# Kernel optimization log

Measured on AMD Instinct MI355X. Metric: run time of the kernel, lower is better.

The kernel has to match this reference:

```python
import jax, jax.numpy as jnp
import numpy as np

DIM = 64
CTX_DIM = 128
B, D, H, W = 4, 64, 64, 64


def setup_inputs() -> dict:
    key = jax.random.key(0)
    ks = jax.random.split(key, 8)
    s_x = 1.0 / np.sqrt(DIM)
    s_c = 1.0 / np.sqrt(CTX_DIM)
    return {
        "x": jax.random.normal(ks[0], (B, DIM, D, H, W), dtype=jnp.float32),
        "context": jax.random.normal(ks[1], (B, CTX_DIM, D, H, W), dtype=jnp.float32),
        # 1x1x1 Conv3d weights flattened to [out_ch, in_ch] plus bias [out_ch]
        "wq": jax.random.uniform(ks[2], (DIM, DIM), jnp.float32, -s_x, s_x),
        "bq": jax.random.uniform(ks[3], (DIM,), jnp.float32, -s_x, s_x),
        "wk": jax.random.uniform(ks[4], (DIM, CTX_DIM), jnp.float32, -s_c, s_c),
        "bk": jax.random.uniform(ks[5], (DIM,), jnp.float32, -s_c, s_c),
        "wv": jax.random.uniform(ks[6], (DIM, CTX_DIM), jnp.float32, -s_c, s_c),
        "bv": jax.random.uniform(ks[7], (DIM,), jnp.float32, -s_c, s_c),
    }


def reference(x, context, wq, bq, wk, bk, wv, bv):
    # 1x1x1 Conv3d == per-voxel channel GEMM
    def conv1(w, b, t):
        return jnp.einsum('oc,bcdhw->bodhw', w, t) + b[None, :, None, None, None]

    scale = x.shape[1] ** (-0.5)
    q = conv1(wq, bq, x)          # [B, dim, D, H, W]
    k = conv1(wk, bk, context)    # [B, dim, D, H, W]
    v = conv1(wv, bv, context)    # [B, dim, D, H, W]

    # (q*scale) @ k^T batched over (B, dim, D): [H,W] @ [W,H] -> [H,H]
    attn = jnp.einsum('bcdhw,bcdgw->bcdhg', q * scale, k)  # [B, dim, D, H, H]
    attn = jax.nn.softmax(attn, axis=-1)
    out = jnp.einsum('bcdhg,bcdgw->bcdhw', attn, v)        # [B, dim, D, H, W]
    return out + x
```

## Files before the change

kernel.cpp:

```cpp
#include <hip/hip_runtime.h>
#include <hip/hip_bf16.h>

typedef short short8 __attribute__((ext_vector_type(8)));
typedef float floatx4 __attribute__((ext_vector_type(4)));
typedef unsigned short ushort_t;

#define NB   4
#define NC_X 64
#define NC_C 128
#define ND   64
#define NHW  4096
#define NH   64
#define NW   64
#define NS   (NB * ND)

__device__ __forceinline__ ushort_t f2bf(float f) {
    unsigned u;
    __builtin_memcpy(&u, &f, 4);
    u += 0x7fffu + ((u >> 16) & 1u);
    return (ushort_t)(u >> 16);
}

__global__ void prep_kernel(const float* __restrict__ wq, const float* __restrict__ bq,
                            const float* __restrict__ wk, const float* __restrict__ bk,
                            const float* __restrict__ wv, const float* __restrict__ bv,
                            ushort_t* __restrict__ wW, float* __restrict__ wB) {
    int t = blockIdx.x * blockDim.x + threadIdx.x;
    int N = gridDim.x * blockDim.x;
    for (int i = t; i < 4096; i += N) wW[i] = f2bf(wq[i] * 0.125f);
    for (int i = t; i < 8192; i += N) wW[4096 + i] = f2bf(wk[i]);
    for (int i = t; i < 8192; i += N) wW[12288 + i] = f2bf(wv[i]);
    for (int i = t; i < 64; i += N) {
        wB[i] = bq[i] * 0.125f;
        wB[64 + i] = bk[i];
        wB[128 + i] = bv[i];
    }
}

__global__ __launch_bounds__(256, 2)
void proj_kernel(const float* __restrict__ x, const float* __restrict__ ctx,
                 const ushort_t* __restrict__ wW, const float* __restrict__ wB,
                 ushort_t* __restrict__ qws, ushort_t* __restrict__ kws,
                 ushort_t* __restrict__ vws, int s0, int nd) {
    __shared__ ushort_t Xs[128][72];
    __shared__ ushort_t Cs[128][136];

    const int t = threadIdx.x;
    const int chunk = blockIdx.x;
    const int si = blockIdx.y;
    const int s = s0 + si;
    const int b = s >> 6;
    const int d = s & 63;
    const int hw0 = chunk * 128;

    const float* xb = x + ((size_t)(b * NC_X) * ND + d) * NHW + hw0;
    const float* cb = ctx + ((size_t)(b * NC_C) * ND + d) * NHW + hw0;

    {
        const int hw = t & 127;
        const int icg0 = (t >> 7) * 4;
        #pragma unroll
        for (int i = 0; i < 4; ++i) {
            const int ic = (icg0 + i) * 8;
            short8 v;
            #pragma unroll
            for (int j = 0; j < 8; ++j)
                v[j] = (short)f2bf(xb[(size_t)(ic + j) * (ND * NHW) + hw]);
            *(short8*)&Xs[hw][ic] = v;
        }
        const int icg0c = (t >> 7) * 8;
        #pragma unroll
        for (int i = 0; i < 8; ++i) {
            const int ic = (icg0c + i) * 8;
            short8 v;
            #pragma unroll
            for (int j = 0; j < 8; ++j)
                v[j] = (short)f2bf(cb[(size_t)(ic + j) * (ND * NHW) + hw]);
            *(short8*)&Cs[hw][ic] = v;
        }
    }
    __syncthreads();

    const int wv = t >> 6, lane = t & 63, l15 = lane & 15, quad = lane >> 4;
    const floatx4 zero4 = {0.f, 0.f, 0.f, 0.f};

    short8 aQ[4][2];
    #pragma unroll
    for (int mt = 0; mt < 4; ++mt)
        #pragma unroll
        for (int kk = 0; kk < 2; ++kk)
            aQ[mt][kk] = *(const short8*)&wW[(mt * 16 + l15) * 64 + kk * 32 + quad * 8];

    floatx4 acc[4][2];
    #pragma unroll
    for (int mt = 0; mt < 4; ++mt)
        #pragma unroll
        for (int n = 0; n < 2; ++n) acc[mt][n] = zero4;

    #pragma unroll
    for (int kk = 0; kk < 2; ++kk) {
        short8 bX[2];
        #pragma unroll
        for (int n = 0; n < 2; ++n)
            bX[n] = *(const short8*)&Xs[(2 * wv + n) * 16 + l15][kk * 32 + quad * 8];
        #pragma unroll
        for (int mt = 0; mt < 4; ++mt)
            #pragma unroll
            for (int n = 0; n < 2; ++n)
                acc[mt][n] = __builtin_amdgcn_mfma_f32_16x16x32_bf16(
                    aQ[mt][kk], bX[n], acc[mt][n], 0, 0, 0);
    }
    #pragma unroll
    for (int mt = 0; mt < 4; ++mt)
        #pragma unroll
        for (int n = 0; n < 2; ++n) {
            const int col = hw0 + (2 * wv + n) * 16 + l15;
            #pragma unroll
            for (int r = 0; r < 4; ++r) {
                const int oc = mt * 16 + quad * 4 + r;
                qws[((size_t)(oc * nd + si)) * NHW + col] = f2bf(acc[mt][n][r] + wB[oc]);
            }
        }

    floatx4 acc2[8][2];
    #pragma unroll
    for (int mt = 0; mt < 8; ++mt)
        #pragma unroll
        for (int n = 0; n < 2; ++n) acc2[mt][n] = zero4;

    #pragma unroll
    for (int kk = 0; kk < 4; ++kk) {
        short8 bC[2];
        #pragma unroll
        for (int n = 0; n < 2; ++n)
            bC[n] = *(const short8*)&Cs[(2 * wv + n) * 16 + l15][kk * 32 + quad * 8];
        #pragma unroll
        for (int mt = 0; mt < 8; ++mt) {
            const short8 aW =
                *(const short8*)&wW[4096 + (mt * 16 + l15) * 128 + kk * 32 + quad * 8];
            #pragma unroll
            for (int n = 0; n < 2; ++n)
                acc2[mt][n] = __builtin_amdgcn_mfma_f32_16x16x32_bf16(
                    aW, bC[n], acc2[mt][n], 0, 0, 0);
        }
    }
    #pragma unroll
    for (int mt = 0; mt < 8; ++mt)
        #pragma unroll
        for (int n = 0; n < 2; ++n) {
            const int col = hw0 + (2 * wv + n) * 16 + l15;
            #pragma unroll
            for (int r = 0; r < 4; ++r) {
                const int row = mt * 16 + quad * 4 + r;
                const float val = acc2[mt][n][r] + wB[64 + row];
                ushort_t* dst = (row < 64) ? kws : vws;
                dst[((size_t)((row & 63) * nd + si)) * NHW + col] = f2bf(val);
            }
        }
}

__global__ __launch_bounds__(256, 3)
void attn_kernel(const ushort_t* __restrict__ qws, const ushort_t* __restrict__ kws,
                 const ushort_t* __restrict__ vws, const float* __restrict__ x,
                 float* __restrict__ out, int s0, int nd) {
    __shared__ ushort_t Vs[64][72];
    __shared__ ushort_t Ps[64][72];

    const int c = blockIdx.x, si = blockIdx.y;
    const int s = s0 + si;
    const int b = s >> 6;
    const int d = s & 63;
    const ushort_t* qp = qws + (size_t)(c * nd + si) * NHW;
    const ushort_t* kp = kws + (size_t)(c * nd + si) * NHW;
    const ushort_t* vp = vws + (size_t)(c * nd + si) * NHW;
    const float* xp = x + ((size_t)(b * NC_X + c) * ND + d) * NHW;
    float* op = out + ((size_t)(b * NC_X + c) * ND + d) * NHW;

    const int t = threadIdx.x;
    const int wv = t >> 6, lane = t & 63, l15 = lane & 15, quad = lane >> 4;

    float xv[4][4];
    #pragma unroll
    for (int nt = 0; nt < 4; ++nt)
        #pragma unroll
        for (int r = 0; r < 4; ++r)
            xv[nt][r] = xp[(wv * 16 + quad * 4 + r) * NW + nt * 16 + l15];

    {
        const int w = t & 63;
        const int gg0 = (t >> 6) * 2;
        #pragma unroll
        for (int i = 0; i < 2; ++i) {
            const int g = (gg0 + i) * 8;
            short8 vvv;
            #pragma unroll
            for (int j = 0; j < 8; ++j) vvv[j] = (short)vp[(g + j) * NW + w];
            *(short8*)&Vs[w][g] = vvv;
        }
    }
    __syncthreads();

    const floatx4 zero4 = {0.f, 0.f, 0.f, 0.f};

    short8 aQ[2], bK[4][2];
    #pragma unroll
    for (int kk = 0; kk < 2; ++kk)
        aQ[kk] = *(const short8*)&qp[(wv * 16 + l15) * NW + kk * 32 + quad * 8];
    #pragma unroll
    for (int nt = 0; nt < 4; ++nt)
        #pragma unroll
        for (int kk = 0; kk < 2; ++kk)
            bK[nt][kk] = *(const short8*)&kp[(nt * 16 + l15) * NW + kk * 32 + quad * 8];

    floatx4 sA[4];
    #pragma unroll
    for (int nt = 0; nt < 4; ++nt) sA[nt] = zero4;
    #pragma unroll
    for (int kk = 0; kk < 2; ++kk)
        #pragma unroll
        for (int nt = 0; nt < 4; ++nt)
            sA[nt] = __builtin_amdgcn_mfma_f32_16x16x32_bf16(aQ[kk], bK[nt][kk], sA[nt], 0, 0, 0);

    float linv[4];
    #pragma unroll
    for (int r = 0; r < 4; ++r) {
        float m = sA[0][r];
        #pragma unroll
        for (int nt = 1; nt < 4; ++nt) m = fmaxf(m, sA[nt][r]);
        #pragma unroll
        for (int off = 1; off < 16; off <<= 1) m = fmaxf(m, __shfl_xor(m, off, 64));
        float e[4], sum = 0.f;
        #pragma unroll
        for (int nt = 0; nt < 4; ++nt) {
            e[nt] = __expf(sA[nt][r] - m);
            sum += e[nt];
        }
        #pragma unroll
        for (int off = 1; off < 16; off <<= 1) sum += __shfl_xor(sum, off, 64);
        linv[r] = 1.0f / sum;
        const int row = wv * 16 + quad * 4 + r;
        #pragma unroll
        for (int nt = 0; nt < 4; ++nt) Ps[row][nt * 16 + l15] = f2bf(e[nt]);
    }
    __syncthreads();

    short8 aP[2], bV[4][2];
    #pragma unroll
    for (int kk = 0; kk < 2; ++kk)
        aP[kk] = *(const short8*)&Ps[wv * 16 + l15][kk * 32 + quad * 8];
    #pragma unroll
    for (int nt = 0; nt < 4; ++nt)
        #pragma unroll
        for (int kk = 0; kk < 2; ++kk)
            bV[nt][kk] = *(const short8*)&Vs[nt * 16 + l15][kk * 32 + quad * 8];

    floatx4 o[4];
    #pragma unroll
    for (int nt = 0; nt < 4; ++nt) o[nt] = zero4;
    #pragma unroll
    for (int kk = 0; kk < 2; ++kk)
        #pragma unroll
        for (int nt = 0; nt < 4; ++nt)
            o[nt] = __builtin_amdgcn_mfma_f32_16x16x32_bf16(aP[kk], bV[nt][kk], o[nt], 0, 0, 0);

    #pragma unroll
    for (int nt = 0; nt < 4; ++nt)
        #pragma unroll
        for (int r = 0; r < 4; ++r) {
            const int row = wv * 16 + quad * 4 + r;
            const int col = nt * 16 + l15;
            op[row * NW + col] = o[nt][r] * linv[r] + xv[nt][r];
        }
}

extern "C" void kernel_launch(void* const* d_in, const int* in_sizes, int n_in,
                              void* d_out, int out_size, void* d_ws, size_t ws_size,
                              hipStream_t stream) {
    const float* x = (const float*)d_in[0];
    const float* ctx = (const float*)d_in[1];
    const float* wq = (const float*)d_in[2];
    const float* bq = (const float*)d_in[3];
    const float* wk = (const float*)d_in[4];
    const float* bk = (const float*)d_in[5];
    const float* wv = (const float*)d_in[6];
    const float* bv = (const float*)d_in[7];
    float* out = (float*)d_out;

    ushort_t* wW = (ushort_t*)d_ws;
    float* wB = (float*)((char*)d_ws + 40960);

    const size_t perSlice = 3ull * NC_X * NHW * 2;
    size_t avail = (ws_size > 65536) ? ws_size - 65536 : perSlice;
    int W = (int)(avail / perSlice);
    if (W > NS) W = NS;
    if (W < 1) W = 1;

    ushort_t* qws = (ushort_t*)((char*)d_ws + 65536);
    ushort_t* kws = qws + (size_t)NC_X * W * NHW;
    ushort_t* vws = kws + (size_t)NC_X * W * NHW;

    prep_kernel<<<dim3(32), dim3(256), 0, stream>>>(wq, bq, wk, bk, wv, bv, wW, wB);

    for (int s0 = 0; s0 < NS; s0 += W) {
        const int w = (NS - s0 < W) ? (NS - s0) : W;
        proj_kernel<<<dim3(32, w), dim3(256), 0, stream>>>(
            x, ctx, wW, wB, qws, kws, vws, s0, w);
        attn_kernel<<<dim3(64, w), dim3(256), 0, stream>>>(
            qws, kws, vws, x, out, s0, w);
    }
}
```

Baseline: 1.238 ms.

## Load projection inputs via direct global-to-LDS copies and overlap V transpose

The projection kernel now stages raw fp32 x/context tiles into shared memory with global_load_lds 16-byte copies using an XOR swizzle, converting to bf16 when reading MFMA operands, and halves the tile width to 64 voxels per block (doubling the grid, raising occupancy hint to 3). This replaces strided scalar global loads with per-element conversion. The attention kernel issues coalesced vector loads of V, Q, K and x up front, runs the QK MFMAs, then transposes V through an extra LDS buffer instead of doing strided global gathers. This costs extra LDS and a second shared-memory pass.

```diff
diff --git a/kernel.cpp b/kernel.cpp
--- a/kernel.cpp
+++ b/kernel.cpp
@@ -19,6 +19,12 @@
     __builtin_memcpy(&u, &f, 4);
     u += 0x7fffu + ((u >> 16) & 1u);
     return (ushort_t)(u >> 16);
+}
+
+__device__ __forceinline__ void gld_lds16(const void* g, void* l) {
+    __builtin_amdgcn_global_load_lds(
+        (const __attribute__((address_space(1))) unsigned int*)g,
+        (__attribute__((address_space(3))) unsigned int*)l, 16, 0, 0);
 }
 
 __global__ void prep_kernel(const float* __restrict__ wq, const float* __restrict__ bq,
@@ -37,52 +43,49 @@
     }
 }
 
-__global__ __launch_bounds__(256, 2)
+__global__ __launch_bounds__(256, 3)
 void proj_kernel(const float* __restrict__ x, const float* __restrict__ ctx,
                  const ushort_t* __restrict__ wW, const float* __restrict__ wB,
                  ushort_t* __restrict__ qws, ushort_t* __restrict__ kws,
                  ushort_t* __restrict__ vws, int s0, int nd) {
-    __shared__ ushort_t Xs[128][72];
-    __shared__ ushort_t Cs[128][136];
+    __shared__ float XF[64 * 64];
+    __shared__ float CF[128 * 64];
 
     const int t = threadIdx.x;
-    const int chunk = blockIdx.x;
     const int si = blockIdx.y;
     const int s = s0 + si;
     const int b = s >> 6;
     const int d = s & 63;
-    const int hw0 = chunk * 128;
+    const int hw0 = blockIdx.x * 64;
 
     const float* xb = x + ((size_t)(b * NC_X) * ND + d) * NHW + hw0;
     const float* cb = ctx + ((size_t)(b * NC_C) * ND + d) * NHW + hw0;
 
+    const int wv = t >> 6, lane = t & 63, l15 = lane & 15, quad = lane >> 4;
+
     {
-        const int hw = t & 127;
-        const int icg0 = (t >> 7) * 4;
-        #pragma unroll
-        for (int i = 0; i < 4; ++i) {
-            const int ic = (icg0 + i) * 8;
-            short8 v;
-            #pragma unroll
-            for (int j = 0; j < 8; ++j)
-                v[j] = (short)f2bf(xb[(size_t)(ic + j) * (ND * NHW) + hw]);
-            *(short8*)&Xs[hw][ic] = v;
-        }
-        const int icg0c = (t >> 7) * 8;
-        #pragma unroll
-        for (int i = 0; i < 8; ++i) {
-            const int ic = (icg0c + i) * 8;
-            short8 v;
-            #pragma unroll
-            for (int j = 0; j < 8; ++j)
-                v[j] = (short)f2bf(cb[(size_t)(ic + j) * (ND * NHW) + hw]);
-            *(short8*)&Cs[hw][ic] = v;
+        const int lr = lane >> 4;
+        const int gs = lane & 15;
+        #pragma unroll
+        for (int i = 0; i < 12; ++i) {
+            const int k = wv * 12 + i;
+            if (k < 16) {
+                const int ic = k * 4 + lr;
+                const int g = gs ^ (((ic >> 3) & 3) << 1);
+                gld_lds16(xb + ((size_t)ic << 18) + g * 4, &XF[k * 256]);
+            } else {
+                const int kc = k - 16;
+                const int ic = kc * 4 + lr;
+                const int g = gs ^ (((ic >> 3) & 3) << 1);
+                gld_lds16(cb + ((size_t)ic << 18) + g * 4, &CF[kc * 256]);
+            }
         }
     }
     __syncthreads();
 
-    const int wv = t >> 6, lane = t & 63, l15 = lane & 15, quad = lane >> 4;
     const floatx4 zero4 = {0.f, 0.f, 0.f, 0.f};
+    const int lo = l15 & 3;
+    const int hb = wv * 4 + (l15 >> 2);
 
     short8 aQ[4][2];
     #pragma unroll
@@ -91,78 +94,69 @@
         for (int kk = 0; kk < 2; ++kk)
             aQ[mt][kk] = *(const short8*)&wW[(mt * 16 + l15) * 64 + kk * 32 + quad * 8];
 
-    floatx4 acc[4][2];
-    #pragma unroll
-    for (int mt = 0; mt < 4; ++mt)
-        #pragma unroll
-        for (int n = 0; n < 2; ++n) acc[mt][n] = zero4;
+    floatx4 acc[4];
+    #pragma unroll
+    for (int mt = 0; mt < 4; ++mt) acc[mt] = zero4;
 
     #pragma unroll
     for (int kk = 0; kk < 2; ++kk) {
-        short8 bX[2];
-        #pragma unroll
-        for (int n = 0; n < 2; ++n)
-            bX[n] = *(const short8*)&Xs[(2 * wv + n) * 16 + l15][kk * 32 + quad * 8];
+        const int sw = ((kk * 4 + quad) & 3) << 1;
+        const float* bb = &XF[(kk * 32 + quad * 8) * 64 + (hb ^ sw) * 4 + lo];
+        short8 bX;
+        #pragma unroll
+        for (int j = 0; j < 8; ++j) bX[j] = (short)f2bf(bb[j * 64]);
         #pragma unroll
         for (int mt = 0; mt < 4; ++mt)
-            #pragma unroll
-            for (int n = 0; n < 2; ++n)
-                acc[mt][n] = __builtin_amdgcn_mfma_f32_16x16x32_bf16(
-                    aQ[mt][kk], bX[n], acc[mt][n], 0, 0, 0);
-    }
-    #pragma unroll
-    for (int mt = 0; mt < 4; ++mt)
-        #pragma unroll
-        for (int n = 0; n < 2; ++n) {
-            const int col = hw0 + (2 * wv + n) * 16 + l15;
+            acc[mt] = __builtin_amdgcn_mfma_f32_16x16x32_bf16(aQ[mt][kk], bX, acc[mt], 0, 0, 0);
+    }
+    {
+        const int col = hw0 + wv * 16 + l15;
+        #pragma unroll
+        for (int mt = 0; mt < 4; ++mt)
             #pragma unroll
             for (int r = 0; r < 4; ++r) {
                 const int oc = mt * 16 + quad * 4 + r;
-                qws[((size_t)(oc * nd + si)) * NHW + col] = f2bf(acc[mt][n][r] + wB[oc]);
+                qws[((size_t)(oc * nd + si)) * NHW + col] = f2bf(acc[mt][r] + wB[oc]);
             }
-        }
-
-    floatx4 acc2[8][2];
-    #pragma unroll
-    for (int mt = 0; mt < 8; ++mt)
-        #pragma unroll
-        for (int n = 0; n < 2; ++n) acc2[mt][n] = zero4;
+    }
+
+    floatx4 acc2[8];
+    #pragma unroll
+    for (int mt = 0; mt < 8; ++mt) acc2[mt] = zero4;
 
     #pragma unroll
     for (int kk = 0; kk < 4; ++kk) {
-        short8 bC[2];
-        #pragma unroll
-        for (int n = 0; n < 2; ++n)
-            bC[n] = *(const short8*)&Cs[(2 * wv + n) * 16 + l15][kk * 32 + quad * 8];
+        const int sw = ((kk * 4 + quad) & 3) << 1;
+        const float* bb = &CF[(kk * 32 + quad * 8) * 64 + (hb ^ sw) * 4 + lo];
+        short8 bC;
+        #pragma unroll
+        for (int j = 0; j < 8; ++j) bC[j] = (short)f2bf(bb[j * 64]);
         #pragma unroll
         for (int mt = 0; mt < 8; ++mt) {
             const short8 aW =
                 *(const short8*)&wW[4096 + (mt * 16 + l15) * 128 + kk * 32 + quad * 8];
-            #pragma unroll
-            for (int n = 0; n < 2; ++n)
-                acc2[mt][n] = __builtin_amdgcn_mfma_f32_16x16x32_bf16(
-                    aW, bC[n], acc2[mt][n], 0, 0, 0);
-        }
-    }
-    #pragma unroll
-    for (int mt = 0; mt < 8; ++mt)
-        #pragma unroll
-        for (int n = 0; n < 2; ++n) {
-            const int col = hw0 + (2 * wv + n) * 16 + l15;
+            acc2[mt] = __builtin_amdgcn_mfma_f32_16x16x32_bf16(aW, bC, acc2[mt], 0, 0, 0);
+        }
+    }
+    {
+        const int col = hw0 + wv * 16 + l15;
+        #pragma unroll
+        for (int mt = 0; mt < 8; ++mt)
             #pragma unroll
             for (int r = 0; r < 4; ++r) {
                 const int row = mt * 16 + quad * 4 + r;
-                const float val = acc2[mt][n][r] + wB[64 + row];
+                const float val = acc2[mt][r] + wB[64 + row];
                 ushort_t* dst = (row < 64) ? kws : vws;
                 dst[((size_t)((row & 63) * nd + si)) * NHW + col] = f2bf(val);
             }
-        }
+    }
 }
 
 __global__ __launch_bounds__(256, 3)
 void attn_kernel(const ushort_t* __restrict__ qws, const ushort_t* __restrict__ kws,
                  const ushort_t* __restrict__ vws, const float* __restrict__ x,
                  float* __restrict__ out, int s0, int nd) {
+    __shared__ ushort_t Vn[64][72];
     __shared__ ushort_t Vs[64][72];
     __shared__ ushort_t Ps[64][72];
 
@@ -179,47 +173,59 @@
     const int t = threadIdx.x;
     const int wv = t >> 6, lane = t & 63, l15 = lane & 15, quad = lane >> 4;
 
+    short8 vreg[2];
+    int vg[2], vw0[2];
+    #pragma unroll
+    for (int i = 0; i < 2; ++i) {
+        const int ch = t + i * 256;
+        vg[i] = ch >> 3;
+        vw0[i] = (ch & 7) * 8;
+        vreg[i] = *(const short8*)&vp[vg[i] * NW + vw0[i]];
+    }
+    short8 aQ[2], bK[4][2];
+    #pragma unroll
+    for (int kk = 0; kk < 2; ++kk)
+        aQ[kk] = *(const short8*)&qp[(wv * 16 + l15) * NW + kk * 32 + quad * 8];
+    #pragma unroll
+    for (int nt = 0; nt < 4; ++nt)
+        #pragma unroll
+        for (int kk = 0; kk < 2; ++kk)
+            bK[nt][kk] = *(const short8*)&kp[(nt * 16 + l15) * NW + kk * 32 + quad * 8];
     float xv[4][4];
     #pragma unroll
     for (int nt = 0; nt < 4; ++nt)
         #pragma unroll
         for (int r = 0; r < 4; ++r)
             xv[nt][r] = xp[(wv * 16 + quad * 4 + r) * NW + nt * 16 + l15];
+
+    const floatx4 zero4 = {0.f, 0.f, 0.f, 0.f};
+
+    floatx4 sA[4];
+    #pragma unroll
+    for (int nt = 0; nt < 4; ++nt) sA[nt] = zero4;
+    #pragma unroll
+    for (int kk = 0; kk < 2; ++kk)
+        #pragma unroll
+        for (int nt = 0; nt < 4; ++nt)
+            sA[nt] = __builtin_amdgcn_mfma_f32_16x16x32_bf16(aQ[kk], bK[nt][kk], sA[nt], 0, 0, 0);
+
+    #pragma unroll
+    for (int i = 0; i < 2; ++i)
+        *(short8*)&Vn[vg[i]][vw0[i]] = vreg[i];
+    __syncthreads();
 
     {
         const int w = t & 63;
         const int gg0 = (t >> 6) * 2;
         #pragma unroll
         for (int i = 0; i < 2; ++i) {
-            const int g = (gg0 + i) * 8;
+            const int g8 = (gg0 + i) * 8;
             short8 vvv;
             #pragma unroll
-            for (int j = 0; j < 8; ++j) vvv[j] = (short)vp[(g + j) * NW + w];
-            *(short8*)&Vs[w][g] = vvv;
-        }
-    }
-    __syncthreads();
-
-    const floatx4 zero4 = {0.f, 0.f, 0.f, 0.f};
-
-    short8 aQ[2], bK[4][2];
-    #pragma unroll
-    for (int kk = 0; kk < 2; ++kk)
-        aQ[kk] = *(const short8*)&qp[(wv * 16 + l15) * NW + kk * 32 + quad * 8];
-    #pragma unroll
-    for (int nt = 0; nt < 4; ++nt)
-        #pragma unroll
-        for (int kk = 0; kk < 2; ++kk)
-            bK[nt][kk] = *(const short8*)&kp[(nt * 16 + l15) * NW + kk * 32 + quad * 8];
-
-    floatx4 sA[4];
-    #pragma unroll
-    for (int nt = 0; nt < 4; ++nt) sA[nt] = zero4;
-    #pragma unroll
-    for (int kk = 0; kk < 2; ++kk)
-        #pragma unroll
-        for (int nt = 0; nt < 4; ++nt)
-            sA[nt] = __builtin_amdgcn_mfma_f32_16x16x32_bf16(aQ[kk], bK[nt][kk], sA[nt], 0, 0, 0);
+            for (int j = 0; j < 8; ++j) vvv[j] = (short)Vn[g8 + j][w];
+            *(short8*)&Vs[w][g8] = vvv;
+        }
+    }
 
     float linv[4];
     #pragma unroll
@@ -303,7 +309,7 @@
 
     for (int s0 = 0; s0 < NS; s0 += W) {
         const int w = (NS - s0 < W) ? (NS - s0) : W;
-        proj_kernel<<<dim3(32, w), dim3(256), 0, stream>>>(
+        proj_kernel<<<dim3(64, w), dim3(256), 0, stream>>>(
             x, ctx, wW, wB, qws, kws, vws, s0, w);
         attn_kernel<<<dim3(64, w), dim3(256), 0, stream>>>(
             qws, kws, vws, x, out, s0, w);
```

Result: slower. 1.451 ms (+17.2%).
